# Performance work log

Measured on AMD Instinct MI355X. Metric: run time of the kernel, lower is better.

The kernel has to match this reference:

```python
import jax, jax.numpy as jnp
import numpy as np

B, T, K = 32, 512, 256


def setup_inputs() -> dict:
    key = jax.random.key(0)
    k1, k2, k3 = jax.random.split(key, 3)
    emissions = jax.random.normal(k1, (B, T, K), dtype=jnp.float32)
    tags = jax.random.randint(k2, (B, T), 0, K)
    mask = jnp.ones((B, T), dtype=jnp.bool_)
    transition_scores = jax.random.normal(k3, (K, K), dtype=jnp.float32)
    return {"emissions": emissions, "tags": tags, "mask": mask,
            "transition_scores": transition_scores}


def _joint_log_likelihood(emissions, tags, mask, trans):
    # emission score at each step: gather emissions[b, t, tags[b, t]]
    maskf = mask.astype(emissions.dtype)  # [B,T]
    emit = jnp.take_along_axis(emissions, tags[:, :, None], axis=2)[..., 0]  # [B,T]
    score = jnp.sum(emit * maskf, axis=1)
    # transition score for steps 1..T-1 (mirrors the torch loop exactly)
    tr = trans[tags[:, :-1], tags[:, 1:]]  # [B,T-1]
    score = score + jnp.sum(tr * maskf[:, 1:], axis=1)
    return score  # [B]


def _log_partition(emissions, mask, trans):
    alpha0 = emissions[:, 0]  # [B,K]

    def step(alpha, xs):
        emit_t, mask_t = xs  # [B,K], [B]
        # alpha[b,i] + trans[i,j] + emit_t[b,j] -> logsumexp over i
        scores = alpha[:, :, None] + trans[None, :, :] + emit_t[:, None, :]
        alpha_t = jax.scipy.special.logsumexp(scores, axis=1)  # [B,K]
        alpha = jnp.where(mask_t[:, None], alpha_t, alpha)
        return alpha, None

    xs = (jnp.swapaxes(emissions[:, 1:], 0, 1),  # [T-1,B,K]
          jnp.swapaxes(mask[:, 1:], 0, 1))       # [T-1,B]
    alpha, _ = jax.lax.scan(step, alpha0, xs)
    return jax.scipy.special.logsumexp(alpha, axis=1)  # [B]


def reference(emissions, tags, mask, transition_scores):
    log_num = _joint_log_likelihood(emissions, tags, mask, transition_scores)
    log_den = _log_partition(emissions, mask, transition_scores)
    return jnp.mean(log_den - log_num)
```

## Files before the change

### kernel.cpp

```cpp
#include <hip/hip_runtime.h>
#include <stdint.h>

#define CB 32
#define CT 512
#define CK 256
#define SHIFT 5.0f
#define NUMOFF (64 + 14 * CB * CK)

typedef _Float16 f16x8 __attribute__((ext_vector_type(8)));
typedef float f32x4 __attribute__((ext_vector_type(4)));

__device__ inline uint32_t pk2(float a, float b) {
    return __builtin_bit_cast(uint32_t,
        __builtin_amdgcn_cvt_pkrtz(__expf(a), __expf(b)));
}

__device__ inline void lds_barrier() {
    asm volatile("s_waitcnt lgkmcnt(0)\n\ts_barrier" ::: "memory");
}

template <int CTRL>
__device__ inline float dpp_maxf(float x) {
    int yi = __builtin_amdgcn_update_dpp(
        __builtin_bit_cast(int, x), __builtin_bit_cast(int, x),
        CTRL, 0xF, 0xF, false);
    return fmaxf(x, __builtin_bit_cast(float, yi));
}

__device__ inline float wave_max(float x) {
    x = dpp_maxf<0x111>(x);
    x = dpp_maxf<0x112>(x);
    x = dpp_maxf<0x114>(x);
    x = dpp_maxf<0x118>(x);
    x = dpp_maxf<0x142>(x);
    x = dpp_maxf<0x143>(x);
    return __builtin_bit_cast(float,
        __builtin_amdgcn_readlane(__builtin_bit_cast(int, x), 63));
}

#define MKB_F(kt, n) f16x8 B_##kt##_##n; {                                   \
    const float* tp = trans + (size_t)((kt) * 32 + ko8) * CK + (colg + (n) * 16); \
    uint4 u_;                                                                \
    u_.x = pk2(tp[0],      tp[CK]);                                          \
    u_.y = pk2(tp[2 * CK], tp[3 * CK]);                                      \
    u_.z = pk2(tp[4 * CK], tp[5 * CK]);                                      \
    u_.w = pk2(tp[6 * CK], tp[7 * CK]);                                      \
    B_##kt##_##n = __builtin_bit_cast(f16x8, u_); }

#define MKB_B(kt, n) f16x8 B_##kt##_##n; {                                   \
    const float* tp = trans + (size_t)(colg + (n) * 16) * CK + ((kt) * 32 + ko8); \
    uint4 u_;                                                                \
    u_.x = pk2(tp[0], tp[1]);                                                \
    u_.y = pk2(tp[2], tp[3]);                                                \
    u_.z = pk2(tp[4], tp[5]);                                                \
    u_.w = pk2(tp[6], tp[7]);                                                \
    B_##kt##_##n = __builtin_bit_cast(f16x8, u_); }

#define LOADB(MK) MK(0,0) MK(0,1) MK(1,0) MK(1,1) MK(2,0) MK(2,1) MK(3,0) MK(3,1) \
                  MK(4,0) MK(4,1) MK(5,0) MK(5,1) MK(6,0) MK(6,1) MK(7,0) MK(7,1)

#define MM(kt)                                                               \
    accA = __builtin_amdgcn_mfma_f32_16x16x32_f16(a##kt##_, B_##kt##_0, accA, 0, 0, 0); \
    accB = __builtin_amdgcn_mfma_f32_16x16x32_f16(a##kt##_, B_##kt##_1, accB, 0, 0, 0);

#define MFMA_STEP(pb)                                                        \
    f16x8 a0_ = *reinterpret_cast<const f16x8*>((pb) + 0   + ko8);           \
    f16x8 a1_ = *reinterpret_cast<const f16x8*>((pb) + 32  + ko8);           \
    f16x8 a2_ = *reinterpret_cast<const f16x8*>((pb) + 64  + ko8);           \
    f16x8 a3_ = *reinterpret_cast<const f16x8*>((pb) + 96  + ko8);           \
    f16x8 a4_ = *reinterpret_cast<const f16x8*>((pb) + 128 + ko8);           \
    f16x8 a5_ = *reinterpret_cast<const f16x8*>((pb) + 160 + ko8);           \
    f16x8 a6_ = *reinterpret_cast<const f16x8*>((pb) + 192 + ko8);           \
    f16x8 a7_ = *reinterpret_cast<const f16x8*>((pb) + 224 + ko8);           \
    f32x4 accA = {0.f, 0.f, 0.f, 0.f};                                       \
    f32x4 accB = {0.f, 0.f, 0.f, 0.f};                                       \
    MM(0) MM(1) MM(2) MM(3) MM(4) MM(5) MM(6) MM(7)

#define FWD_RUN(T_LO, T_HI, AJ_INIT, OUTP) {                                 \
    LOADB(MKB_F)                                                             \
    float aj = (AJ_INIT);                                                    \
    float emit_next = emB[(size_t)(T_LO) * CK + sj];                         \
    {   const float mw = wave_max(aj);                                       \
        if (l == 0) wmaxl[0][w] = mw; }                                      \
    __syncthreads();                                                         \
    float Mref;                                                              \
    {   const float4 wa = *reinterpret_cast<const float4*>(&wmaxl[0][0]);    \
        const float4 wb = *reinterpret_cast<const float4*>(&wmaxl[0][4]);    \
        Mref = fmaxf(fmaxf(fmaxf(wa.x, wa.y), fmaxf(wa.z, wa.w)),            \
                     fmaxf(fmaxf(wb.x, wb.y), fmaxf(wb.z, wb.w))) + SHIFT; } \
    __syncthreads();                                                         \
    for (int t = (T_LO); t <= (T_HI); ++t) {                                 \
        const float emit_t = emit_next;                                      \
        const int nxt = (t + 1 <= (T_HI)) ? (t + 1) : (T_HI);                \
        emit_next = emB[(size_t)nxt * CK + sj];                              \
        const int bsel = t & 1;                                              \
        const float mw = wave_max(aj);                                       \
        if (l == 0) wmaxl[bsel][w] = mw;                                     \
        const float pv = __expf(aj - Mref);                                  \
        if (l < 32) pbuf[bsel][w * 32 + l] = (_Float16)pv;                   \
        lds_barrier();                                                       \
        const float4 wa = *reinterpret_cast<const float4*>(&wmaxl[bsel][0]); \
        const float4 wb = *reinterpret_cast<const float4*>(&wmaxl[bsel][4]); \
        const float Mnext = fmaxf(fmaxf(fmaxf(wa.x, wa.y), fmaxf(wa.z, wa.w)), \
                                  fmaxf(fmaxf(wb.x, wb.y), fmaxf(wb.z, wb.w))) + SHIFT; \
        MFMA_STEP(pbuf[bsel])                                                \
        const float s = nsel ? accB[0] : accA[0];                            \
        const float anew = Mref + __logf(s) + emit_t;                        \
        aj = (mask_lds[t] != 0.f) ? anew : aj;                               \
        Mref = Mnext;                                                        \
    }                                                                        \
    if (l < 32) (OUTP)[w * 32 + l] = aj; }

#define BWD_RUN(TN_LO, TN_HI, OUTP) {                                        \
    LOADB(MKB_B)                                                             \
    float bj = 0.f;                                                          \
    float emit_next = emB[(size_t)(TN_HI) * CK + sj];                        \
    __syncthreads();                                                         \
    {   const float mw = wave_max(bj + emit_next);                           \
        if (l == 0) wmaxl[0][w] = mw; }                                      \
    __syncthreads();                                                         \
    float Mref;                                                              \
    {   const float4 wa = *reinterpret_cast<const float4*>(&wmaxl[0][0]);    \
        const float4 wb = *reinterpret_cast<const float4*>(&wmaxl[0][4]);    \
        Mref = fmaxf(fmaxf(fmaxf(wa.x, wa.y), fmaxf(wa.z, wa.w)),            \
                     fmaxf(fmaxf(wb.x, wb.y), fmaxf(wb.z, wb.w))) + SHIFT; } \
    __syncthreads();                                                         \
    for (int tn = (TN_HI); tn >= (TN_LO); --tn) {                            \
        const float emit_t = emit_next;                                      \
        const int nxt = (tn - 1 > (TN_LO)) ? (tn - 1) : (TN_LO);             \
        emit_next = emB[(size_t)nxt * CK + sj];                              \
        const int bsel = tn & 1;                                             \
        const float v = bj + emit_t;                                         \
        const float mw = wave_max(v);                                        \
        if (l == 0) wmaxl[bsel][w] = mw;                                     \
        const float pv = __expf(v - Mref);                                   \
        if (l < 32) pbuf[bsel][w * 32 + l] = (_Float16)pv;                   \
        lds_barrier();                                                       \
        const float4 wa = *reinterpret_cast<const float4*>(&wmaxl[bsel][0]); \
        const float4 wb = *reinterpret_cast<const float4*>(&wmaxl[bsel][4]); \
        const float Mnext = fmaxf(fmaxf(fmaxf(wa.x, wa.y), fmaxf(wa.z, wa.w)), \
                                  fmaxf(fmaxf(wb.x, wb.y), fmaxf(wb.z, wb.w))) + SHIFT; \
        MFMA_STEP(pbuf[bsel])                                                \
        const float s = nsel ? accB[0] : accA[0];                            \
        const float bnew = Mref + __logf(s);                                 \
        bj = (mask_lds[tn] != 0.f) ? bnew : bj;                              \
        Mref = Mnext;                                                        \
    }                                                                        \
    if (l < 32) (OUTP)[w * 32 + l] = bj; }

__global__ __launch_bounds__(512, 1) void crf_seg_kernel(
    const float* __restrict__ emissions,
    const int* __restrict__ tags,
    const int* __restrict__ mask,
    const float* __restrict__ trans,
    float* __restrict__ ws)
{
    const int tid = threadIdx.x;
    const int w = tid >> 6;
    const int l = tid & 63;
    const int ko8 = ((l >> 4) & 3) * 8;
    const int colg = w * 32 + (l & 15);
    const int nsel = (l >> 4) & 1;
    const int sj = w * 32 + nsel * 16 + (l & 15);
    const int grp = blockIdx.x >> 5;
    const int b = blockIdx.x & 31;

    __shared__ __align__(16) _Float16 pbuf[2][CK];
    __shared__ __align__(16) float wmaxl[2][8];
    __shared__ float mask_lds[CT];

    const float* emB = emissions + (size_t)b * CT * CK;
    const int* tagB = tags + b * CT;
    const int* maskB = mask + b * CT;
    mask_lds[tid] = maskB[tid] ? 1.f : 0.f;

    if (tid < 64) {
        const int t = 64 * grp + l;
        const float mf = maskB[t] ? 1.f : 0.f;
        float num = emB[(size_t)t * CK + tagB[t]] * mf;
        if (t >= 1) num += trans[(size_t)tagB[t - 1] * CK + tagB[t]] * mf;
        #pragma unroll
        for (int off = 32; off > 0; off >>= 1) num += __shfl_down(num, off, 64);
        if (l == 0) ws[NUMOFF + grp * CB + b] = num;
    }

    const int lo1 = (grp == 0) ? 1 : (64 * grp + 1);
    const int hi1 = (grp == 7) ? 511 : (64 * grp + 64);
    const int slot1 = (grp == 0) ? 0 : (6 + grp);
    float* const out1 = ws + 64 + (size_t)slot1 * CB * CK + (size_t)b * CK;

    if (grp == 0) {
        FWD_RUN(1, 64, emB[sj], out1)
    } else {
        BWD_RUN(lo1, hi1, out1)
    }

    if (grp <= 5) {
        const int phi = 64 * (grp + 2);
        const int plo = phi - 2;
        float* const out2 = ws + 64 + (size_t)(grp + 1) * CB * CK + (size_t)b * CK;
        __syncthreads();
        FWD_RUN(plo, phi, 0.f, out2)
    }
}

__device__ inline float block_lse(float v, float* red, int tid) {
    const int wid = tid >> 6, lane = tid & 63;
    float mx = v;
    #pragma unroll
    for (int off = 32; off > 0; off >>= 1) mx = fmaxf(mx, __shfl_down(mx, off, 64));
    mx = __shfl(mx, 0, 64);
    if (lane == 0) red[wid] = mx;
    __syncthreads();
    const float g = fmaxf(fmaxf(red[0], red[1]), fmaxf(red[2], red[3]));
    float ex = __expf(v - g);
    #pragma unroll
    for (int off = 32; off > 0; off >>= 1) ex += __shfl_down(ex, off, 64);
    if (lane == 0) red[4 + wid] = ex;
    __syncthreads();
    const float r = g + __logf(red[4] + red[5] + red[6] + red[7]);
    __syncthreads();
    return r;
}

__global__ void crf_combine_kernel(float* __restrict__ ws) {
    const int b = blockIdx.x;
    const int tid = threadIdx.x;
    __shared__ float red[8];

    if (tid == 0) {
        float num = 0.f;
        #pragma unroll
        for (int g = 0; g < 8; ++g) num += ws[NUMOFF + g * CB + b];
        ws[CB + b] = num;
    }

    const float* base = ws + 64;
    float r;
    {
        const float FA1 = base[0 * CB * CK + b * CK + tid];
        const float FB1 = base[7 * CB * CK + b * CK + tid];
        r = block_lse(FA1 + FB1, red, tid);
    }
    #pragma unroll
    for (int k = 2; k <= 7; ++k) {
        const float FAk = base[(size_t)(k - 1) * CB * CK + b * CK + tid];
        const float FBk = base[(size_t)(6 + k) * CB * CK + b * CK + tid];
        r += block_lse(FAk + FBk, red, tid);
        r -= block_lse(FAk, red, tid);
    }
    if (tid == 0) ws[b] = r;
}

__global__ void crf_finalize_kernel(const float* __restrict__ ws,
                                    float* __restrict__ out) {
    float v = 0.f;
    if ((int)threadIdx.x < CB) v = ws[threadIdx.x] - ws[CB + threadIdx.x];
    #pragma unroll
    for (int off = 32; off > 0; off >>= 1) v += __shfl_down(v, off, 64);
    if (threadIdx.x == 0) out[0] = v * (1.f / CB);
}

extern "C" void kernel_launch(void* const* d_in, const int* in_sizes, int n_in,
                              void* d_out, int out_size, void* d_ws, size_t ws_size,
                              hipStream_t stream) {
    const float* emissions = (const float*)d_in[0];
    const int* tags = (const int*)d_in[1];
    const int* mask = (const int*)d_in[2];
    const float* trans = (const float*)d_in[3];
    float* out = (float*)d_out;
    float* ws = (float*)d_ws;

    crf_seg_kernel<<<8 * CB, 512, 0, stream>>>(emissions, tags, mask, trans, ws);
    crf_combine_kernel<<<CB, 256, 0, stream>>>(ws);
    crf_finalize_kernel<<<1, 64, 0, stream>>>(ws, out);
}
```

Measured before the change: 68.27 us.

## Pack two sequence-segment groups into one 1024-thread block

Each block now runs two independent 512-thread sub-blocks, each handling its own time segment, so the grid shrinks from 256 to 128 blocks. The LDS scratch buffers are split per sub-block, and an extra trailing barrier is meant to balance barrier counts between the two halves. The aim is to pack more waves onto each CU to hide the latency of the serial recurrence and to cut block count. The cost is that block-wide barriers now couple both halves every step, and fewer CUs are occupied.

```diff
diff --git a/kernel.cpp b/kernel.cpp
--- a/kernel.cpp
+++ b/kernel.cpp
@@ -81,11 +81,11 @@
     float aj = (AJ_INIT);                                                    \
     float emit_next = emB[(size_t)(T_LO) * CK + sj];                         \
     {   const float mw = wave_max(aj);                                       \
-        if (l == 0) wmaxl[0][w] = mw; }                                      \
+        if (l == 0) wmaxlS[0][w] = mw; }                                     \
     __syncthreads();                                                         \
     float Mref;                                                              \
-    {   const float4 wa = *reinterpret_cast<const float4*>(&wmaxl[0][0]);    \
-        const float4 wb = *reinterpret_cast<const float4*>(&wmaxl[0][4]);    \
+    {   const float4 wa = *reinterpret_cast<const float4*>(&wmaxlS[0][0]);   \
+        const float4 wb = *reinterpret_cast<const float4*>(&wmaxlS[0][4]);   \
         Mref = fmaxf(fmaxf(fmaxf(wa.x, wa.y), fmaxf(wa.z, wa.w)),            \
                      fmaxf(fmaxf(wb.x, wb.y), fmaxf(wb.z, wb.w))) + SHIFT; } \
     __syncthreads();                                                         \
@@ -95,15 +95,15 @@
         emit_next = emB[(size_t)nxt * CK + sj];                              \
         const int bsel = t & 1;                                              \
         const float mw = wave_max(aj);                                       \
-        if (l == 0) wmaxl[bsel][w] = mw;                                     \
+        if (l == 0) wmaxlS[bsel][w] = mw;                                    \
         const float pv = __expf(aj - Mref);                                  \
-        if (l < 32) pbuf[bsel][w * 32 + l] = (_Float16)pv;                   \
+        if (l < 32) pbufS[bsel][w * 32 + l] = (_Float16)pv;                  \
         lds_barrier();                                                       \
-        const float4 wa = *reinterpret_cast<const float4*>(&wmaxl[bsel][0]); \
-        const float4 wb = *reinterpret_cast<const float4*>(&wmaxl[bsel][4]); \
+        const float4 wa = *reinterpret_cast<const float4*>(&wmaxlS[bsel][0]);\
+        const float4 wb = *reinterpret_cast<const float4*>(&wmaxlS[bsel][4]);\
         const float Mnext = fmaxf(fmaxf(fmaxf(wa.x, wa.y), fmaxf(wa.z, wa.w)), \
                                   fmaxf(fmaxf(wb.x, wb.y), fmaxf(wb.z, wb.w))) + SHIFT; \
-        MFMA_STEP(pbuf[bsel])                                                \
+        MFMA_STEP(pbufS[bsel])                                               \
         const float s = nsel ? accB[0] : accA[0];                            \
         const float anew = Mref + __logf(s) + emit_t;                        \
         aj = (mask_lds[t] != 0.f) ? anew : aj;                               \
@@ -117,11 +117,11 @@
     float emit_next = emB[(size_t)(TN_HI) * CK + sj];                        \
     __syncthreads();                                                         \
     {   const float mw = wave_max(bj + emit_next);                           \
-        if (l == 0) wmaxl[0][w] = mw; }                                      \
+        if (l == 0) wmaxlS[0][w] = mw; }                                     \
     __syncthreads();                                                         \
     float Mref;                                                              \
-    {   const float4 wa = *reinterpret_cast<const float4*>(&wmaxl[0][0]);    \
-        const float4 wb = *reinterpret_cast<const float4*>(&wmaxl[0][4]);    \
+    {   const float4 wa = *reinterpret_cast<const float4*>(&wmaxlS[0][0]);   \
+        const float4 wb = *reinterpret_cast<const float4*>(&wmaxlS[0][4]);   \
         Mref = fmaxf(fmaxf(fmaxf(wa.x, wa.y), fmaxf(wa.z, wa.w)),            \
                      fmaxf(fmaxf(wb.x, wb.y), fmaxf(wb.z, wb.w))) + SHIFT; } \
     __syncthreads();                                                         \
@@ -132,15 +132,15 @@
         const int bsel = tn & 1;                                             \
         const float v = bj + emit_t;                                         \
         const float mw = wave_max(v);                                        \
-        if (l == 0) wmaxl[bsel][w] = mw;                                     \
+        if (l == 0) wmaxlS[bsel][w] = mw;                                    \
         const float pv = __expf(v - Mref);                                   \
-        if (l < 32) pbuf[bsel][w * 32 + l] = (_Float16)pv;                   \
+        if (l < 32) pbufS[bsel][w * 32 + l] = (_Float16)pv;                  \
         lds_barrier();                                                       \
-        const float4 wa = *reinterpret_cast<const float4*>(&wmaxl[bsel][0]); \
-        const float4 wb = *reinterpret_cast<const float4*>(&wmaxl[bsel][4]); \
+        const float4 wa = *reinterpret_cast<const float4*>(&wmaxlS[bsel][0]);\
+        const float4 wb = *reinterpret_cast<const float4*>(&wmaxlS[bsel][4]);\
         const float Mnext = fmaxf(fmaxf(fmaxf(wa.x, wa.y), fmaxf(wa.z, wa.w)), \
                                   fmaxf(fmaxf(wb.x, wb.y), fmaxf(wb.z, wb.w))) + SHIFT; \
-        MFMA_STEP(pbuf[bsel])                                                \
+        MFMA_STEP(pbufS[bsel])                                               \
         const float s = nsel ? accB[0] : accA[0];                            \
         const float bnew = Mref + __logf(s);                                 \
         bj = (mask_lds[tn] != 0.f) ? bnew : bj;                              \
@@ -148,7 +148,7 @@
     }                                                                        \
     if (l < 32) (OUTP)[w * 32 + l] = bj; }
 
-__global__ __launch_bounds__(512, 1) void crf_seg_kernel(
+__global__ __launch_bounds__(1024, 1) void crf_seg_kernel(
     const float* __restrict__ emissions,
     const int* __restrict__ tags,
     const int* __restrict__ mask,
@@ -156,25 +156,31 @@
     float* __restrict__ ws)
 {
     const int tid = threadIdx.x;
-    const int w = tid >> 6;
+    const int sub = tid >> 9;
+    const int t5 = tid & 511;
+    const int w = t5 >> 6;
     const int l = tid & 63;
     const int ko8 = ((l >> 4) & 3) * 8;
     const int colg = w * 32 + (l & 15);
     const int nsel = (l >> 4) & 1;
     const int sj = w * 32 + nsel * 16 + (l & 15);
-    const int grp = blockIdx.x >> 5;
+    const int pair = blockIdx.x >> 5;
     const int b = blockIdx.x & 31;
-
-    __shared__ __align__(16) _Float16 pbuf[2][CK];
-    __shared__ __align__(16) float wmaxl[2][8];
+    const int grp = pair * 2 + sub;
+
+    __shared__ __align__(16) _Float16 pbuf[2][2][CK];
+    __shared__ __align__(16) float wmaxl[2][2][8];
     __shared__ float mask_lds[CT];
+
+    _Float16 (*const pbufS)[CK] = pbuf[sub];
+    float (*const wmaxlS)[8] = wmaxl[sub];
 
     const float* emB = emissions + (size_t)b * CT * CK;
     const int* tagB = tags + b * CT;
     const int* maskB = mask + b * CT;
-    mask_lds[tid] = maskB[tid] ? 1.f : 0.f;
-
-    if (tid < 64) {
+    if (tid < CT) mask_lds[tid] = maskB[tid] ? 1.f : 0.f;
+
+    if (t5 < 64) {
         const int t = 64 * grp + l;
         const float mf = maskB[t] ? 1.f : 0.f;
         float num = emB[(size_t)t * CK + tagB[t]] * mf;
@@ -202,6 +208,8 @@
         __syncthreads();
         FWD_RUN(plo, phi, 0.f, out2)
     }
+
+    if (grp == 0 || grp == 7) __syncthreads();
 }
 
 __device__ inline float block_lse(float v, float* red, int tid) {
@@ -271,7 +279,7 @@
     float* out = (float*)d_out;
     float* ws = (float*)d_ws;
 
-    crf_seg_kernel<<<8 * CB, 512, 0, stream>>>(emissions, tags, mask, trans, ws);
+    crf_seg_kernel<<<4 * CB, 1024, 0, stream>>>(emissions, tags, mask, trans, ws);
     crf_combine_kernel<<<CB, 256, 0, stream>>>(ws);
     crf_finalize_kernel<<<1, 64, 0, stream>>>(ws, out);
 }
```

After: 128.7 us. 88.5% more time.
